# Performance work log

Hardware: AMD Instinct MI355X
Metric: run time of the kernel (lower is better)

The kernel has to match this reference:

```python
import jax, jax.numpy as jnp
import numpy as np

N, K, D = 131072, 1024, 128


def setup_inputs() -> dict:
    key = jax.random.key(0)
    k1, k2 = jax.random.split(key)
    latent = jax.random.normal(k1, (N, D), dtype=jnp.float32)
    coords = jax.random.uniform(k2, (K, D), dtype=jnp.float32)  # torch.rand init
    return {"latent": latent, "coords": coords}


def reference(latent, coords):
    # Euclidean cdist argmin: sqrt is monotone, so argmin of squared distances
    # matches torch.cdist(...).min(1)[1].
    x2 = jnp.sum(latent * latent, axis=1, keepdims=True)          # [N, 1]
    c2 = jnp.sum(coords * coords, axis=1)[None, :]                # [1, K]
    d2 = x2 + c2 - 2.0 * (latent @ coords.T)                      # [N, K]
    closest_centroid = jnp.argmin(d2, axis=1)                     # [N] int
    # original also computes cluster_distances but discards it; output is indices
    return closest_centroid
```

## Files before the change

### kernel.cpp

```cpp
#include <hip/hip_runtime.h>


constexpr int N = 131072;
constexpr int K = 1024;
constexpr int D = 128;

typedef __attribute__((ext_vector_type(8))) _Float16 half8;
typedef __attribute__((ext_vector_type(4))) float f32x4;

typedef const __attribute__((address_space(1))) uint* gas_uint;
typedef __attribute__((address_space(3))) uint* las_uint;

union UH { uint4 u; half8 h; };
__device__ inline half8 as_h8(uint4 v) { UH x; x.u = v; return x.h; }

union H2U { _Float16 h[2]; uint u; };
__device__ inline uint fp16pk(float a, float b) {
    H2U x;
    x.h[0] = (_Float16)a;
    x.h[1] = (_Float16)b;
    return x.u;
}
__device__ inline void fp16split(float a, _Float16& hi, _Float16& lo) {
    hi = (_Float16)a;
    lo = (_Float16)(a - (float)hi);
}
__device__ inline void pk2(float a, float b, uint& h, uint& l) {
    _Float16 ha, la, hb, lb;
    fp16split(a, ha, la);
    fp16split(b, hb, lb);
    H2U x, y;
    x.h[0] = ha; x.h[1] = hb;
    y.h[0] = la; y.h[1] = lb;
    h = x.u;
    l = y.u;
}

__global__ __launch_bounds__(256) void prep_kernel(
    const float* __restrict__ coords, float* __restrict__ c2half,
    uint* __restrict__ chi, int* __restrict__ counter) {
    if (blockIdx.x == 0 && threadIdx.x == 0) counter[0] = 0;
    const int k = blockIdx.x * 4 + (threadIdx.x >> 6);
    const int dw = threadIdx.x & 63;
    float a = coords[k * D + 2 * dw], b = coords[k * D + 2 * dw + 1];
    const int g = dw >> 2, sub = dw & 3, kt = k >> 5, m = k & 31;
    char* base = (char*)chi + (size_t)kt * 8192 + m * 256 +
                 ((g ^ (m & 15)) << 4) + sub * 4;
    *(uint*)base = fp16pk(a, b);
    float s = fmaf(a, a, b * b);
#pragma unroll
    for (int off = 1; off < 64; off <<= 1) s += __shfl_xor(s, off);
    if (dw == 0) c2half[k] = 0.5f * s;
}

__global__ __launch_bounds__(256) void transpose_kernel(
    const float* __restrict__ coords, float* __restrict__ coordsT) {
    __shared__ float tile[64][65];
    const int k0 = blockIdx.x * 64;
    const int d0 = blockIdx.y * 64;
    const int tx = threadIdx.x & 63, ty = threadIdx.x >> 6;
#pragma unroll
    for (int i = 0; i < 64; i += 4)
        tile[ty + i][tx] = coords[(size_t)(k0 + ty + i) * D + d0 + tx];
    __syncthreads();
#pragma unroll
    for (int i = 0; i < 64; i += 4)
        coordsT[(size_t)(d0 + ty + i) * K + k0 + tx] = tile[tx][ty + i];
}

__global__ __launch_bounds__(64, 2) void centroid_mfma_kernel(
    const float* __restrict__ latent, const uint* __restrict__ chi,
    const float* __restrict__ c2, int* __restrict__ out,
    int* __restrict__ counter, int* __restrict__ list) {
    __shared__ __align__(16) char smem[20480];
    const int l = threadIdx.x;
    const int l15 = l & 15, l4 = l >> 4;
    const int rowbase = blockIdx.x * 64;

    uint4 bh[4][4], bl[4][4];
    float n2[4];
#pragma unroll
    for (int grp = 0; grp < 4; ++grp) {
        const float* rp =
            latent + (size_t)(rowbase + grp * 16 + l15) * D + l4 * 8;
        float s2 = 0.f;
#pragma unroll
        for (int s = 0; s < 4; ++s) {
            float4 u = *(const float4*)(rp + 32 * s);
            float4 v = *(const float4*)(rp + 32 * s + 4);
            s2 += u.x * u.x + u.y * u.y + u.z * u.z + u.w * u.w +
                  v.x * v.x + v.y * v.y + v.z * v.z + v.w * v.w;
            uint h0, o0, h1, o1, h2, o2, h3, o3;
            pk2(-u.x, -u.y, h0, o0);
            pk2(-u.z, -u.w, h1, o1);
            pk2(-v.x, -v.y, h2, o2);
            pk2(-v.z, -v.w, h3, o3);
            bh[grp][s] = make_uint4(h0, h1, h2, h3);
            bl[grp][s] = make_uint4(o0, o1, o2, o3);
        }
        n2[grp] = s2;
    }
#pragma unroll
    for (int grp = 0; grp < 4; ++grp) {
        n2[grp] += __shfl_xor(n2[grp], 16);
        n2[grp] += __shfl_xor(n2[grp], 32);
    }

    {
        float4* dst = (float4*)(smem + 16384);
        const float4* src = (const float4*)c2;
#pragma unroll
        for (int i = 0; i < 4; ++i) dst[i * 64 + l] = src[i * 64 + l];
    }

    const char* gsrc0 = (const char*)chi + (l << 4);
#pragma unroll
    for (int i = 0; i < 8; ++i)
        __builtin_amdgcn_global_load_lds((gas_uint)(gsrc0 + i * 1024),
                                         (las_uint)(smem + i * 1024), 16, 0, 0);
#pragma unroll
    for (int i = 0; i < 8; ++i)
        __builtin_amdgcn_global_load_lds((gas_uint)(gsrc0 + 8192 + i * 1024),
                                         (las_uint)(smem + 8192 + i * 1024),
                                         16, 0, 0);

    float m1[4] = {3.4e38f, 3.4e38f, 3.4e38f, 3.4e38f};
    float m2[4] = {3.4e38f, 3.4e38f, 3.4e38f, 3.4e38f};
    uint kpack[8];
#pragma unroll
    for (int ks = 0; ks < 2; ++ks)
#pragma unroll
        for (int r = 0; r < 4; ++r) kpack[ks * 4 + r] = ks * 16 + l4 * 4 + r;
    const float* c2l = (const float*)(smem + 16384);

#pragma unroll 1
    for (int t = 0; t < 32; ++t) {
        const int buf = t & 1;
        if (t < 31)
            asm volatile("s_waitcnt vmcnt(8)" ::: "memory");
        else
            asm volatile("s_waitcnt vmcnt(0)" ::: "memory");
        __builtin_amdgcn_sched_barrier(0);

        const int k0 = t * 32;
        f32x4 acc[2][4];
#pragma unroll
        for (int ks = 0; ks < 2; ++ks) {
            float4 cq = *(const float4*)(c2l + k0 + ks * 16 + l4 * 4);
#pragma unroll
            for (int grp = 0; grp < 4; ++grp) {
                acc[ks][grp][0] = cq.x;
                acc[ks][grp][1] = cq.y;
                acc[ks][grp][2] = cq.z;
                acc[ks][grp][3] = cq.w;
            }
        }

        const char* lhs = smem + buf * 8192;
        __builtin_amdgcn_s_setprio(1);
#pragma unroll
        for (int s = 0; s < 4; ++s) {
            half8 a[2];
#pragma unroll
            for (int ks = 0; ks < 2; ++ks) {
                const int m = ks * 16 + l15;
                const int g = l4 + 4 * s;
                a[ks] = *(const half8*)(lhs + m * 256 + ((g ^ (m & 15)) << 4));
            }
#pragma unroll
            for (int ks = 0; ks < 2; ++ks)
#pragma unroll
                for (int grp = 0; grp < 4; ++grp) {
                    acc[ks][grp] = __builtin_amdgcn_mfma_f32_16x16x32_f16(
                        a[ks], as_h8(bh[grp][s]), acc[ks][grp], 0, 0, 0);
                    acc[ks][grp] = __builtin_amdgcn_mfma_f32_16x16x32_f16(
                        a[ks], as_h8(bl[grp][s]), acc[ks][grp], 0, 0, 0);
                }
        }
        __builtin_amdgcn_s_setprio(0);
        __builtin_amdgcn_sched_barrier(0);

#pragma unroll
        for (int ks = 0; ks < 2; ++ks) {
#pragma unroll
            for (int r = 0; r < 4; ++r) {
                const uint kk = kpack[ks * 4 + r];
#pragma unroll
                for (int grp = 0; grp < 4; ++grp) {
                    uint pb = (__float_as_uint(acc[ks][grp][r]) & 0xFFFFFC00u) | kk;
                    float vp = __uint_as_float(pb);
                    m2[grp] = __builtin_amdgcn_fmed3f(vp, m1[grp], m2[grp]);
                    m1[grp] = fminf(m1[grp], vp);
                }
            }
        }
#pragma unroll
        for (int i = 0; i < 8; ++i) kpack[i] += 32;

        asm volatile("s_waitcnt lgkmcnt(0)" ::: "memory");
        __builtin_amdgcn_sched_barrier(0);
        if (t < 30) {
            const char* gs = gsrc0 + (size_t)(t + 2) * 8192;
            char* ls = smem + buf * 8192;
#pragma unroll
            for (int i = 0; i < 8; ++i)
                __builtin_amdgcn_global_load_lds((gas_uint)(gs + i * 1024),
                                                 (las_uint)(ls + i * 1024),
                                                 16, 0, 0);
        }
    }

#pragma unroll
    for (int off = 16; off <= 32; off <<= 1) {
#pragma unroll
        for (int grp = 0; grp < 4; ++grp) {
            float om = __shfl_xor(m1[grp], off);
            float o2 = __shfl_xor(m2[grp], off);
            m2[grp] = fminf(fminf(m2[grp], o2), fmaxf(m1[grp], om));
            m1[grp] = fminf(m1[grp], om);
        }
    }

    bool flg[4];
    unsigned long long bm[4];
    int total = 0;
#pragma unroll
    for (int grp = 0; grp < 4; ++grp) {
        float eps = 0.0028f * sqrtf(n2[grp]) + 0.015f;
        flg[grp] = (l < 16) && ((m2[grp] - m1[grp]) <= eps);
        bm[grp] = __ballot(flg[grp]);
        total += __popcll(bm[grp]);
    }
    int pos = 0;
    if (l == 0 && total) pos = atomicAdd(counter, total);
    pos = __shfl(pos, 0);
    if (l < 16) {
        int run = pos;
#pragma unroll
        for (int grp = 0; grp < 4; ++grp) {
            out[rowbase + grp * 16 + l] = (int)(__float_as_uint(m1[grp]) & 1023u);
            if (flg[grp])
                list[run + __popcll(bm[grp] & ((1ull << l) - 1ull))] =
                    rowbase + grp * 16 + l;
            run += __popcll(bm[grp]);
        }
    }
}

__global__ __launch_bounds__(256) void centroid_exact_kernel(
    const float* __restrict__ latent, const float* __restrict__ coordsT,
    const float* __restrict__ c2, const int* __restrict__ cnt_list,
    int* __restrict__ out) {
    const int count = cnt_list[0];
    const int* list = cnt_list + 16;
    const int lane = threadIdx.x & 63;
    const int gw = (blockIdx.x * 256 + threadIdx.x) >> 6;
    const int nwaves = gridDim.x * 4;

    for (int task = gw; task * 4 < count; task += nwaves) {
        const int base = task * 4;
        const int nr = min(4, count - base);
        const float* xp[4];
        int rows[4];
#pragma unroll
        for (int j = 0; j < 4; ++j) {
            int idx = base + (j < nr ? j : nr - 1);
            rows[j] = __builtin_amdgcn_readfirstlane(list[idx]);
            xp[j] = latent + (size_t)rows[j] * D;
        }

        float acc[16][4];
#pragma unroll
        for (int c = 0; c < 16; ++c) {
            float cc = c2[c * 64 + lane];
#pragma unroll
            for (int j = 0; j < 4; ++j) acc[c][j] = cc;
        }

#pragma unroll 1
        for (int d4 = 0; d4 < D / 4; ++d4) {
            float4 xq[4];
#pragma unroll
            for (int j = 0; j < 4; ++j)
                xq[j] = *(const float4*)(xp[j] + 4 * d4);
            float ct[4][16];
#pragma unroll
            for (int dd = 0; dd < 4; ++dd)
#pragma unroll
                for (int c = 0; c < 16; ++c)
                    ct[dd][c] = coordsT[(size_t)(4 * d4 + dd) * K + c * 64 + lane];
#pragma unroll
            for (int dd = 0; dd < 4; ++dd) {
#pragma unroll
                for (int c = 0; c < 16; ++c) {
#pragma unroll
                    for (int j = 0; j < 4; ++j) {
                        float xv = (dd == 0) ? xq[j].x
                                 : (dd == 1) ? xq[j].y
                                 : (dd == 2) ? xq[j].z : xq[j].w;
                        acc[c][j] = fmaf(-xv, ct[dd][c], acc[c][j]);
                    }
                }
            }
        }

#pragma unroll
        for (int j = 0; j < 4; ++j) {
            float m1 = acc[0][j];
            int i1 = lane;
#pragma unroll
            for (int c = 1; c < 16; ++c) {
                const int kk = c * 64 + lane;
                if (acc[c][j] < m1) { m1 = acc[c][j]; i1 = kk; }
            }
#pragma unroll
            for (int off = 1; off < 64; off <<= 1) {
                float om = __shfl_xor(m1, off);
                int oi = __shfl_xor(i1, off);
                if (om < m1 || (om == m1 && oi < i1)) { m1 = om; i1 = oi; }
            }
            if (lane == 0 && j < nr) out[rows[j]] = i1;
        }
    }
}

extern "C" void kernel_launch(void* const* d_in, const int* in_sizes, int n_in,
                              void* d_out, int out_size, void* d_ws, size_t ws_size,
                              hipStream_t stream) {
    const float* latent = (const float*)d_in[0];
    const float* coords = (const float*)d_in[1];
    int* out = (int*)d_out;

    char* ws = (char*)d_ws;
    size_t off = 0;
    float* c2 = (float*)(ws + off); off += 4096;
    uint* chi = (uint*)(ws + off); off += 262144;
    float* coordsT = (float*)(ws + off); off += 524288;
    int* cnt_list = (int*)(ws + off); off += 64 + 524288;
    int* counter = cnt_list;
    int* list = cnt_list + 16;

    prep_kernel<<<K / 4, 256, 0, stream>>>(coords, c2, chi, counter);
    {
        dim3 g(K / 64, D / 64);
        transpose_kernel<<<g, 256, 0, stream>>>(coords, coordsT);
    }
    centroid_mfma_kernel<<<N / 64, 64, 0, stream>>>(latent, chi, c2, out,
                                                    counter, list);
    centroid_exact_kernel<<<2048, 256, 0, stream>>>(latent, coordsT, c2,
                                                    cnt_list, out);
}
```

Before: 131.4 us.

## Shrink MFMA tile to 32 rows by 16 centroids for higher occupancy

```diff
diff --git a/kernel.cpp b/kernel.cpp
--- a/kernel.cpp
+++ b/kernel.cpp
@@ -43,9 +43,9 @@
     const int k = blockIdx.x * 4 + (threadIdx.x >> 6);
     const int dw = threadIdx.x & 63;
     float a = coords[k * D + 2 * dw], b = coords[k * D + 2 * dw + 1];
-    const int g = dw >> 2, sub = dw & 3, kt = k >> 5, m = k & 31;
-    char* base = (char*)chi + (size_t)kt * 8192 + m * 256 +
-                 ((g ^ (m & 15)) << 4) + sub * 4;
+    const int g = dw >> 2, sub = dw & 3, kt = k >> 4, m = k & 15;
+    char* base = (char*)chi + (size_t)kt * 4096 + m * 256 +
+                 ((g ^ m) << 4) + sub * 4;
     *(uint*)base = fp16pk(a, b);
     float s = fmaf(a, a, b * b);
 #pragma unroll
@@ -68,19 +68,19 @@
         coordsT[(size_t)(d0 + ty + i) * K + k0 + tx] = tile[tx][ty + i];
 }
 
-__global__ __launch_bounds__(64, 2) void centroid_mfma_kernel(
+__global__ __launch_bounds__(64, 4) void centroid_mfma_kernel(
     const float* __restrict__ latent, const uint* __restrict__ chi,
     const float* __restrict__ c2, int* __restrict__ out,
     int* __restrict__ counter, int* __restrict__ list) {
-    __shared__ __align__(16) char smem[20480];
+    __shared__ __align__(16) char smem[12288];
     const int l = threadIdx.x;
     const int l15 = l & 15, l4 = l >> 4;
-    const int rowbase = blockIdx.x * 64;
-
-    uint4 bh[4][4], bl[4][4];
-    float n2[4];
-#pragma unroll
-    for (int grp = 0; grp < 4; ++grp) {
+    const int rowbase = blockIdx.x * 32;
+
+    uint4 bh[2][4], bl[2][4];
+    float n2[2];
+#pragma unroll
+    for (int grp = 0; grp < 2; ++grp) {
         const float* rp =
             latent + (size_t)(rowbase + grp * 16 + l15) * D + l4 * 8;
         float s2 = 0.f;
@@ -101,13 +101,13 @@
         n2[grp] = s2;
     }
 #pragma unroll
-    for (int grp = 0; grp < 4; ++grp) {
+    for (int grp = 0; grp < 2; ++grp) {
         n2[grp] += __shfl_xor(n2[grp], 16);
         n2[grp] += __shfl_xor(n2[grp], 32);
     }
 
     {
-        float4* dst = (float4*)(smem + 16384);
+        float4* dst = (float4*)(smem + 8192);
         const float4* src = (const float4*)c2;
 #pragma unroll
         for (int i = 0; i < 4; ++i) dst[i * 64 + l] = src[i * 64 + l];
@@ -115,95 +115,76 @@
 
     const char* gsrc0 = (const char*)chi + (l << 4);
 #pragma unroll
-    for (int i = 0; i < 8; ++i)
+    for (int i = 0; i < 4; ++i)
         __builtin_amdgcn_global_load_lds((gas_uint)(gsrc0 + i * 1024),
                                          (las_uint)(smem + i * 1024), 16, 0, 0);
 #pragma unroll
-    for (int i = 0; i < 8; ++i)
-        __builtin_amdgcn_global_load_lds((gas_uint)(gsrc0 + 8192 + i * 1024),
-                                         (las_uint)(smem + 8192 + i * 1024),
+    for (int i = 0; i < 4; ++i)
+        __builtin_amdgcn_global_load_lds((gas_uint)(gsrc0 + 4096 + i * 1024),
+                                         (las_uint)(smem + 4096 + i * 1024),
                                          16, 0, 0);
 
-    float m1[4] = {3.4e38f, 3.4e38f, 3.4e38f, 3.4e38f};
-    float m2[4] = {3.4e38f, 3.4e38f, 3.4e38f, 3.4e38f};
-    uint kpack[8];
-#pragma unroll
-    for (int ks = 0; ks < 2; ++ks)
-#pragma unroll
-        for (int r = 0; r < 4; ++r) kpack[ks * 4 + r] = ks * 16 + l4 * 4 + r;
-    const float* c2l = (const float*)(smem + 16384);
+    float m1[2] = {3.4e38f, 3.4e38f};
+    float m2[2] = {3.4e38f, 3.4e38f};
+    const float* c2l = (const float*)(smem + 8192);
+    float4 cq = *(const float4*)(c2l + l4 * 4);
 
 #pragma unroll 1
-    for (int t = 0; t < 32; ++t) {
+    for (int t = 0; t < 64; ++t) {
         const int buf = t & 1;
-        if (t < 31)
-            asm volatile("s_waitcnt vmcnt(8)" ::: "memory");
+        if (t < 63)
+            asm volatile("s_waitcnt vmcnt(4)" ::: "memory");
         else
             asm volatile("s_waitcnt vmcnt(0)" ::: "memory");
         __builtin_amdgcn_sched_barrier(0);
 
-        const int k0 = t * 32;
-        f32x4 acc[2][4];
-#pragma unroll
-        for (int ks = 0; ks < 2; ++ks) {
-            float4 cq = *(const float4*)(c2l + k0 + ks * 16 + l4 * 4);
-#pragma unroll
-            for (int grp = 0; grp < 4; ++grp) {
-                acc[ks][grp][0] = cq.x;
-                acc[ks][grp][1] = cq.y;
-                acc[ks][grp][2] = cq.z;
-                acc[ks][grp][3] = cq.w;
-            }
-        }
-
-        const char* lhs = smem + buf * 8192;
+        f32x4 acc[2];
+#pragma unroll
+        for (int grp = 0; grp < 2; ++grp) {
+            acc[grp][0] = cq.x;
+            acc[grp][1] = cq.y;
+            acc[grp][2] = cq.z;
+            acc[grp][3] = cq.w;
+        }
+        if (t + 1 < 64) cq = *(const float4*)(c2l + (t + 1) * 16 + l4 * 4);
+
+        const char* lhs = smem + buf * 4096;
         __builtin_amdgcn_s_setprio(1);
 #pragma unroll
         for (int s = 0; s < 4; ++s) {
-            half8 a[2];
-#pragma unroll
-            for (int ks = 0; ks < 2; ++ks) {
-                const int m = ks * 16 + l15;
-                const int g = l4 + 4 * s;
-                a[ks] = *(const half8*)(lhs + m * 256 + ((g ^ (m & 15)) << 4));
-            }
-#pragma unroll
-            for (int ks = 0; ks < 2; ++ks)
-#pragma unroll
-                for (int grp = 0; grp < 4; ++grp) {
-                    acc[ks][grp] = __builtin_amdgcn_mfma_f32_16x16x32_f16(
-                        a[ks], as_h8(bh[grp][s]), acc[ks][grp], 0, 0, 0);
-                    acc[ks][grp] = __builtin_amdgcn_mfma_f32_16x16x32_f16(
-                        a[ks], as_h8(bl[grp][s]), acc[ks][grp], 0, 0, 0);
-                }
+            half8 a = *(const half8*)(lhs + l15 * 256 + (((l4 + 4 * s) ^ l15) << 4));
+            acc[0] = __builtin_amdgcn_mfma_f32_16x16x32_f16(a, as_h8(bh[0][s]),
+                                                            acc[0], 0, 0, 0);
+            acc[1] = __builtin_amdgcn_mfma_f32_16x16x32_f16(a, as_h8(bh[1][s]),
+                                                            acc[1], 0, 0, 0);
+            acc[0] = __builtin_amdgcn_mfma_f32_16x16x32_f16(a, as_h8(bl[0][s]),
+                                                            acc[0], 0, 0, 0);
+            acc[1] = __builtin_amdgcn_mfma_f32_16x16x32_f16(a, as_h8(bl[1][s]),
+                                                            acc[1], 0, 0, 0);
         }
         __builtin_amdgcn_s_setprio(0);
         __builtin_amdgcn_sched_barrier(0);
 
-#pragma unroll
-        for (int ks = 0; ks < 2; ++ks) {
-#pragma unroll
-            for (int r = 0; r < 4; ++r) {
-                const uint kk = kpack[ks * 4 + r];
-#pragma unroll
-                for (int grp = 0; grp < 4; ++grp) {
-                    uint pb = (__float_as_uint(acc[ks][grp][r]) & 0xFFFFFC00u) | kk;
-                    float vp = __uint_as_float(pb);
-                    m2[grp] = __builtin_amdgcn_fmed3f(vp, m1[grp], m2[grp]);
-                    m1[grp] = fminf(m1[grp], vp);
-                }
+        const uint kbase = ((uint)t << 4) + l4 * 4;
+#pragma unroll
+        for (int r = 0; r < 4; ++r) {
+#pragma unroll
+            for (int grp = 0; grp < 2; ++grp) {
+                uint pb = (__float_as_uint(acc[grp][r]) & 0xFFFFFC00u) |
+                          (kbase + r);
+                float vp = __uint_as_float(pb);
+                m2[grp] = __builtin_amdgcn_fmed3f(vp, m1[grp], m2[grp]);
+                m1[grp] = fminf(m1[grp], vp);
             }
         }
-#pragma unroll
-        for (int i = 0; i < 8; ++i) kpack[i] += 32;
 
         asm volatile("s_waitcnt lgkmcnt(0)" ::: "memory");
         __builtin_amdgcn_sched_barrier(0);
-        if (t < 30) {
-            const char* gs = gsrc0 + (size_t)(t + 2) * 8192;
-            char* ls = smem + buf * 8192;
-#pragma unroll
-            for (int i = 0; i < 8; ++i)
+        if (t < 62) {
+            const char* gs = gsrc0 + (size_t)(t + 2) * 4096;
+            char* ls = smem + buf * 4096;
+#pragma unroll
+            for (int i = 0; i < 4; ++i)
                 __builtin_amdgcn_global_load_lds((gas_uint)(gs + i * 1024),
                                                  (las_uint)(ls + i * 1024),
                                                  16, 0, 0);
@@ -213,7 +194,7 @@
 #pragma unroll
     for (int off = 16; off <= 32; off <<= 1) {
 #pragma unroll
-        for (int grp = 0; grp < 4; ++grp) {
+        for (int grp = 0; grp < 2; ++grp) {
             float om = __shfl_xor(m1[grp], off);
             float o2 = __shfl_xor(m2[grp], off);
             m2[grp] = fminf(fminf(m2[grp], o2), fmaxf(m1[grp], om));
@@ -221,11 +202,11 @@
         }
     }
 
-    bool flg[4];
-    unsigned long long bm[4];
+    bool flg[2];
+    unsigned long long bm[2];
     int total = 0;
 #pragma unroll
-    for (int grp = 0; grp < 4; ++grp) {
+    for (int grp = 0; grp < 2; ++grp) {
         float eps = 0.0028f * sqrtf(n2[grp]) + 0.015f;
         flg[grp] = (l < 16) && ((m2[grp] - m1[grp]) <= eps);
         bm[grp] = __ballot(flg[grp]);
@@ -237,7 +218,7 @@
     if (l < 16) {
         int run = pos;
 #pragma unroll
-        for (int grp = 0; grp < 4; ++grp) {
+        for (int grp = 0; grp < 2; ++grp) {
             out[rowbase + grp * 16 + l] = (int)(__float_as_uint(m1[grp]) & 1023u);
             if (flg[grp])
                 list[run + __popcll(bm[grp] & ((1ull << l) - 1ull))] =
@@ -345,7 +326,7 @@
         dim3 g(K / 64, D / 64);
         transpose_kernel<<<g, 256, 0, stream>>>(coords, coordsT);
     }
-    centroid_mfma_kernel<<<N / 64, 64, 0, stream>>>(latent, chi, c2, out,
+    centroid_mfma_kernel<<<N / 32, 64, 0, stream>>>(latent, chi, c2, out,
                                                     counter, list);
     centroid_exact_kernel<<<2048, 256, 0, stream>>>(latent, coordsT, c2,
                                                     cnt_list, out);
```

Result: slower. 162.7 us (+23.9%).
